# Kernel tuning notes

Hardware: AMD Instinct MI355X
Metric: run time of the kernel (lower is better)

Reference implementation:

```python
import jax, jax.numpy as jnp
import numpy as np

D_MODEL = 1024
H = 16
D_K = D_MODEL // H
THETA = 10000.0
MAX_SEQ = 2048
SEQ = 2048
BATCH = 2


def _rope_tables():
    # tri[i, k] angles: i / theta**(2k/d_k)
    pos = jnp.arange(MAX_SEQ, dtype=jnp.float32)[:, None]          # [S, 1]
    inv_freq = THETA ** (-2.0 * jnp.arange(D_K // 2, dtype=jnp.float32) / D_K)  # [dk/2]
    ang = pos * inv_freq                                            # [S, dk/2]
    return jnp.cos(ang), jnp.sin(ang)


def _apply_rope(x, token_positions, cos_t, sin_t):
    # x: [b, h, s, dk]; rotate interleaved pairs
    cos = cos_t[token_positions]  # [s, dk/2]
    sin = sin_t[token_positions]
    x2 = x.reshape(x.shape[:-1] + (D_K // 2, 2))
    x0, x1 = x2[..., 0], x2[..., 1]
    r0 = x0 * cos - x1 * sin
    r1 = x0 * sin + x1 * cos
    return jnp.stack([r0, r1], axis=-1).reshape(x.shape)


def setup_inputs() -> dict:
    key = jax.random.key(0)
    ks = jax.random.split(key, 5)
    sigma = np.sqrt(2.0 / (D_MODEL + D_MODEL))
    return {
        "x": jax.random.normal(ks[0], (BATCH, SEQ, D_MODEL), dtype=jnp.float32),
        "token_positions": jnp.arange(SEQ, dtype=jnp.int64 if jax.config.jax_enable_x64 else jnp.int32),
        "Wq": (jax.random.normal(ks[1], (D_MODEL, D_MODEL), dtype=jnp.float32) * sigma),
        "Wk": (jax.random.normal(ks[2], (D_MODEL, D_MODEL), dtype=jnp.float32) * sigma),
        "Wv": (jax.random.normal(ks[3], (D_MODEL, D_MODEL), dtype=jnp.float32) * sigma),
        "Wo": (jax.random.normal(ks[4], (D_MODEL, D_MODEL), dtype=jnp.float32) * sigma),
    }


def reference(x, token_positions, Wq, Wk, Wv, Wo):
    b, s, _ = x.shape
    cos_t, sin_t = _rope_tables()

    def proj(W):
        y = jnp.einsum('oi,bsi->bso', W, x)                 # [b, s, d_model]
        return y.reshape(b, s, H, D_K).transpose(0, 2, 1, 3)  # [b, h, s, dk]

    Q = _apply_rope(proj(Wq), token_positions, cos_t, sin_t)
    K = _apply_rope(proj(Wk), token_positions, cos_t, sin_t)
    V = proj(Wv)

    scores = jnp.einsum('bhqd,bhkd->bhqk', Q, K) / jnp.sqrt(jnp.float32(D_K))
    causal = jnp.tril(jnp.ones((s, s), dtype=bool))
    scores = jnp.where(causal, scores, -jnp.inf)
    attn = jax.nn.softmax(scores, axis=-1)
    out = jnp.einsum('bhqk,bhkd->bhqd', attn, V)            # [b, h, s, dv]
    out = out.transpose(0, 2, 1, 3).reshape(b, s, D_MODEL)
    return jnp.einsum('oi,bsi->bso', Wo, out)
```

## Files before the change

### kernel.cpp

```cpp
#include <hip/hip_runtime.h>
#include <hip/hip_bf16.h>
#include <math.h>

#define D_MODEL 1024
#define NH      16
#define DK      64
#define SEQ     2048
#define BATCH   2

typedef float  f32x4  __attribute__((ext_vector_type(4)));
typedef __bf16 bf16x8 __attribute__((ext_vector_type(8)));
typedef unsigned short ushx4 __attribute__((ext_vector_type(4)));
typedef unsigned short ushx8 __attribute__((ext_vector_type(8)));
typedef unsigned short u16;

__device__ inline u16 cbf(float f) { __bf16 h = (__bf16)f; return *(u16*)&h; }

__device__ inline void gload16(const u16* g, u16* l) {
    __builtin_amdgcn_global_load_lds(
        (const __attribute__((address_space(1))) unsigned int*)g,
        (__attribute__((address_space(3))) unsigned int*)l,
        16, 0, 0);
}

__global__ void rope_tables_kernel(float2* __restrict__ cs) {
    int i = blockIdx.x * 256 + threadIdx.x;
    int pos = i >> 5, k = i & 31;
    float inv = powf(10000.0f, -2.0f * (float)k / 64.0f);
    float ang = (float)pos * inv;
    cs[i] = make_float2(cosf(ang), sinf(ang));
}

__global__ void cvt_kernel(const float* __restrict__ in, u16* __restrict__ out) {
    size_t i = ((size_t)blockIdx.x * 256 + threadIdx.x) * 8;
    f32x4 v0 = *(const f32x4*)(in + i);
    f32x4 v1 = *(const f32x4*)(in + i + 4);
    ushx4 o0, o1;
    #pragma unroll
    for (int e = 0; e < 4; e++) { o0[e] = cbf(v0[e]); o1[e] = cbf(v1[e]); }
    *(ushx4*)(out + i) = o0;
    *(ushx4*)(out + i + 4) = o1;
}

__global__ void cvtw_kernel(const float* __restrict__ wq, const float* __restrict__ wk,
                            const float* __restrict__ wv, const float* __restrict__ wo,
                            u16* __restrict__ oq, u16* __restrict__ ok,
                            u16* __restrict__ ov, u16* __restrict__ oo) {
    const float* in; u16* out;
    switch (blockIdx.y) {
        case 0: in = wq; out = oq; break;
        case 1: in = wk; out = ok; break;
        case 2: in = wv; out = ov; break;
        default: in = wo; out = oo; break;
    }
    size_t i = ((size_t)blockIdx.x * 256 + threadIdx.x) * 8;
    f32x4 v0 = *(const f32x4*)(in + i);
    f32x4 v1 = *(const f32x4*)(in + i + 4);
    ushx4 o0, o1;
    #pragma unroll
    for (int e = 0; e < 4; e++) { o0[e] = cbf(v0[e]); o1[e] = cbf(v1[e]); }
    *(ushx4*)(out + i) = o0;
    *(ushx4*)(out + i + 4) = o1;
}

template<int MODE>
__global__ __launch_bounds__(256) void gemm_bt(
    const u16* __restrict__ A, const u16* __restrict__ W,
    u16* __restrict__ Qo, u16* __restrict__ Ko, void* __restrict__ Oo,
    const int* __restrict__ tpos, const float2* __restrict__ cs)
{
    constexpr int K = 1024;
    __shared__ u16 As[2][128 * 32];
    __shared__ u16 Bs[2][128 * 32];

    const int t  = threadIdx.x;
    const int m0 = blockIdx.x * 128, n0 = blockIdx.y * 128;
    const int lane = t & 63, wid = t >> 6;
    const int wm = wid >> 1, wn = wid & 1;
    const int lr = lane & 15, lg = lane >> 4;

    const int ldrow0 = wid * 32 + (lane >> 2);
    const int ldrow1 = ldrow0 + 16;
    const int lc = lane & 3;
    const u16* Asrc0 = A + (size_t)(m0 + ldrow0) * K + ((lc ^ ((ldrow0 >> 1) & 3)) << 3);
    const u16* Asrc1 = A + (size_t)(m0 + ldrow1) * K + ((lc ^ ((ldrow1 >> 1) & 3)) << 3);
    const u16* Bsrc0 = W + (size_t)(n0 + ldrow0) * K + ((lc ^ ((ldrow0 >> 1) & 3)) << 3);
    const u16* Bsrc1 = W + (size_t)(n0 + ldrow1) * K + ((lc ^ ((ldrow1 >> 1) & 3)) << 3);
    const int d0 = (wid * 32) * 32, d1 = (wid * 32 + 16) * 32;

    f32x4 acc[4][4];
    #pragma unroll
    for (int i = 0; i < 4; i++)
        #pragma unroll
        for (int j2 = 0; j2 < 4; j2++) acc[i][j2] = 0.0f;

    auto stage = [&](int buf, int k0) {
        gload16(Asrc0 + k0, &As[buf][d0]);
        gload16(Asrc1 + k0, &As[buf][d1]);
        gload16(Bsrc0 + k0, &Bs[buf][d0]);
        gload16(Bsrc1 + k0, &Bs[buf][d1]);
    };

    stage(0, 0);
    int buf = 0;
    for (int k0 = 0; k0 < K; k0 += 32) {
        __syncthreads();
        if (k0 + 32 < K) stage(buf ^ 1, k0 + 32);

        bf16x8 af[4], bfr[4];
        #pragma unroll
        for (int mi = 0; mi < 4; mi++) {
            int row = wm * 64 + mi * 16 + lr;
            af[mi] = *(const bf16x8*)&As[buf][row * 32 + ((lg ^ ((row >> 1) & 3)) << 3)];
        }
        #pragma unroll
        for (int ni = 0; ni < 4; ni++) {
            int row = wn * 64 + ni * 16 + lr;
            bfr[ni] = *(const bf16x8*)&Bs[buf][row * 32 + ((lg ^ ((row >> 1) & 3)) << 3)];
        }
        #pragma unroll
        for (int mi = 0; mi < 4; mi++)
            #pragma unroll
            for (int ni = 0; ni < 4; ni++) {
                if constexpr (MODE == 3)
                    acc[mi][ni] = __builtin_amdgcn_mfma_f32_16x16x32_bf16(bfr[ni], af[mi], acc[mi][ni], 0, 0, 0);
                else
                    acc[mi][ni] = __builtin_amdgcn_mfma_f32_16x16x32_bf16(af[mi], bfr[ni], acc[mi][ni], 0, 0, 0);
            }
        buf ^= 1;
    }

    #pragma unroll
    for (int mi = 0; mi < 4; mi++)
        #pragma unroll
        for (int ni = 0; ni < 4; ni++) {
            f32x4 v4 = acc[mi][ni];
            #pragma unroll
            for (int r = 0; r < 4; r++) {
                float v = v4[r];
                if constexpr (MODE == 3) {
                    int n = n0 + wn * 64 + ni * 16 + lg * 4 + r;
                    int m = m0 + wm * 64 + mi * 16 + lr;
                    int h = n >> 6, d = n & 63;
                    int b = m >> 11, s = m & 2047;
                    ((u16*)Oo)[(((size_t)b * NH + h) * DK + d) * SEQ + s] = cbf(v);
                } else {
                    int m = m0 + wm * 64 + mi * 16 + lg * 4 + r;
                    int n = n0 + wn * 64 + ni * 16 + lr;
                    if constexpr (MODE == 2) {
                        ((float*)Oo)[(size_t)m * D_MODEL + n] = v;
                    } else {
                        int b = m >> 11, s = m & 2047;
                        int h = (n >> 6) & 15, d = n & 63;
                        float vp = __shfl_xor(v, 1);
                        int tp = tpos[s];
                        float2 c2 = cs[tp * 32 + (d >> 1)];
                        float res = (d & 1) ? (vp * c2.y + v * c2.x) : (v * c2.x - vp * c2.y);
                        const int sel = n0 >> 10;
                        if (sel == 0) res *= 0.18033688f;
                        u16* outp = sel ? Ko : Qo;
                        outp[(((size_t)b * NH + h) * SEQ + s) * DK + d] = cbf(res);
                    }
                }
            }
        }
}

__global__ __launch_bounds__(256) void attn_kernel(
    const u16* __restrict__ Q,
    const u16* __restrict__ Km,
    const u16* __restrict__ VT,
    u16* __restrict__ aout)
{
    __shared__ u16 Ks[2][64 * 64];
    __shared__ u16 Vs[64 * 64];
    __shared__ u16 Pl[4][16 * 64];
    const int t = threadIdx.x, wid = t >> 6, lane = t & 63;
    const int lr = lane & 15, lg = lane >> 4;
    const int bx = blockIdx.x;
    const int j = bx & 31;
    const int qb = 31 - (bx >> 5);
    const int bh = (j & 7) * 4 + (j >> 3);
    const int b = bh >> 4, h = bh & 15;
    const int q0 = qb * 64;
    const int qw = q0 + wid * 16;
    const int nkt = qb + 1;
    const int srow = lane >> 3, schunk = lane & 7;

    const u16* Qg = Q  + (size_t)bh * SEQ * DK;
    const u16* Kg = Km + (size_t)bh * SEQ * DK;
    const u16* Vg = VT + (size_t)bh * DK * SEQ;
    u16* Plw = Pl[wid];

    bf16x8 aq[2];
    #pragma unroll
    for (int h2 = 0; h2 < 2; h2++)
        aq[h2] = *(const bf16x8*)&Qg[(qw + lr) * DK + h2 * 32 + lg * 8];

    float m_run = -__builtin_inff(), l_run = 0.0f;
    f32x4 acc[4];
    #pragma unroll
    for (int dg = 0; dg < 4; dg++) acc[dg] = 0.0f;

    auto stageK = [&](int buf, int kb) {
        const int row0 = wid * 16;
        const u16* ks = Kg + (size_t)(kb + row0 + srow) * DK + ((schunk ^ srow) << 3);
        gload16(ks,          &Ks[buf][row0 * 64]);
        gload16(ks + 8 * DK, &Ks[buf][(row0 + 8) * 64]);
    };
    auto stageV = [&](int kb) {
        const int row0 = wid * 16;
        const u16* vs = Vg + (size_t)(row0 + srow) * SEQ + kb + ((schunk ^ srow) << 3);
        gload16(vs,                   &Vs[row0 * 64]);
        gload16(vs + (size_t)8 * SEQ, &Vs[(row0 + 8) * 64]);
    };

    stageK(0, 0);
    for (int kt = 0; kt < nkt; kt++) {
        __builtin_amdgcn_sched_barrier(0);
        __builtin_amdgcn_s_barrier();
        __builtin_amdgcn_sched_barrier(0);
        stageV(kt * 64);
        stageK((kt + 1) & 1, (kt + 1 < nkt) ? (kt + 1) * 64 : 0);
        const int kb = kt * 64;

        asm volatile("s_waitcnt vmcnt(4)" ::: "memory");
        __builtin_amdgcn_sched_barrier(0);
        bf16x8 kf[4][2];
        #pragma unroll
        for (int kg = 0; kg < 4; kg++)
            #pragma unroll
            for (int h2 = 0; h2 < 2; h2++) {
                int row = kg * 16 + lr;
                kf[kg][h2] = *(const bf16x8*)&Ks[kt & 1][row * 64 + (((h2 * 4 + lg) ^ (lr & 7)) << 3)];
            }

        f32x4 sf[4];
        #pragma unroll
        for (int kg = 0; kg < 4; kg++) sf[kg] = 0.0f;
        __builtin_amdgcn_s_setprio(1);
        #pragma unroll
        for (int kg = 0; kg < 4; kg++) {
            sf[kg] = __builtin_amdgcn_mfma_f32_16x16x32_bf16(kf[kg][0], aq[0], sf[kg], 0, 0, 0);
            sf[kg] = __builtin_amdgcn_mfma_f32_16x16x32_bf16(kf[kg][1], aq[1], sf[kg], 0, 0, 0);
        }
        __builtin_amdgcn_s_setprio(0);

        {
            if (kb + 64 > qw) {
                const int qq = qw + lr;
                #pragma unroll
                for (int kg = 0; kg < 4; kg++)
                    #pragma unroll
                    for (int r = 0; r < 4; r++)
                        if (kb + kg * 16 + lg * 4 + r > qq) sf[kg][r] = -__builtin_inff();
            }
            float cmax = sf[0][0];
            #pragma unroll
            for (int kg = 0; kg < 4; kg++)
                #pragma unroll
                for (int r = 0; r < 4; r++) cmax = fmaxf(cmax, sf[kg][r]);
            if (!__all(cmax <= m_run + 8.0f)) {
                float mt = fmaxf(cmax, __shfl_xor(cmax, 16));
                mt = fmaxf(mt, __shfl_xor(mt, 32));
                float mn = fmaxf(m_run, mt);
                float scr = exp2f(m_run - mn);
                m_run = mn;
                l_run *= scr;
                #pragma unroll
                for (int dg = 0; dg < 4; dg++) acc[dg] *= scr;
            }
            float l = 0.0f;
            const int prow = lr * 64;
            #pragma unroll
            for (int kg = 0; kg < 4; kg++) {
                ushx4 pk;
                #pragma unroll
                for (int r = 0; r < 4; r++) {
                    float p = exp2f(sf[kg][r] - m_run);
                    l += p;
                    pk[r] = cbf(p);
                }
                *(ushx4*)&Plw[prow + (((kg * 4 + lg) ^ ((lr & 7) << 1)) << 2)] = pk;
            }
            l_run += l;
        }

        asm volatile("s_waitcnt vmcnt(2)" ::: "memory");
        __builtin_amdgcn_sched_barrier(0);
        bf16x8 vf[2][4];
        #pragma unroll
        for (int ck = 0; ck < 2; ck++)
            #pragma unroll
            for (int dg = 0; dg < 4; dg++) {
                int row = dg * 16 + lr;
                vf[ck][dg] = *(const bf16x8*)&Vs[row * 64 + (((ck * 4 + lg) ^ (lr & 7)) << 3)];
            }

        asm volatile("s_waitcnt lgkmcnt(0)" ::: "memory");
        __builtin_amdgcn_sched_barrier(0);
        bf16x8 pa[2];
        #pragma unroll
        for (int ck = 0; ck < 2; ck++)
            pa[ck] = *(const bf16x8*)&Plw[lr * 64 + (((ck * 8 + lg * 2) ^ ((lr & 7) << 1)) << 2)];
        __builtin_amdgcn_s_setprio(1);
        #pragma unroll
        for (int ck = 0; ck < 2; ck++)
            #pragma unroll
            for (int dg = 0; dg < 4; dg++)
                acc[dg] = __builtin_amdgcn_mfma_f32_16x16x32_bf16(vf[ck][dg], pa[ck], acc[dg], 0, 0, 0);
        __builtin_amdgcn_s_setprio(0);
    }

    l_run += __shfl_xor(l_run, 16);
    l_run += __shfl_xor(l_run, 32);

    {
        float inv = 1.0f / l_run;
        int q = qw + lr;
        #pragma unroll
        for (int dg = 0; dg < 4; dg++) {
            ushx4 ow;
            #pragma unroll
            for (int r = 0; r < 4; r++) ow[r] = cbf(acc[dg][r] * inv);
            *(ushx4*)&aout[((size_t)b * SEQ + q) * D_MODEL + h * DK + dg * 16 + lg * 4] = ow;
        }
    }
}

extern "C" void kernel_launch(void* const* d_in, const int* in_sizes, int n_in,
                              void* d_out, int out_size, void* d_ws, size_t ws_size,
                              hipStream_t stream) {
    const float* x    = (const float*)d_in[0];
    const int*   tpos = (const int*)d_in[1];
    const float* Wq   = (const float*)d_in[2];
    const float* Wk   = (const float*)d_in[3];
    const float* Wv   = (const float*)d_in[4];
    const float* Wo   = (const float*)d_in[5];
    float* out = (float*)d_out;

    char* ws = (char*)d_ws;
    float2* cs = (float2*)ws;
    u16* Qb   = (u16*)(ws + (512 << 10));
    u16* Kb   = (u16*)(ws + (512 << 10) + ((size_t)8  << 20));
    u16* VT   = (u16*)(ws + (512 << 10) + ((size_t)16 << 20));
    u16* xb   = (u16*)(ws + (512 << 10) + ((size_t)24 << 20));
    u16* Wqb  = (u16*)(ws + (512 << 10) + ((size_t)32 << 20));
    u16* Wkb  = (u16*)(ws + (512 << 10) + ((size_t)34 << 20));
    u16* Wvb  = (u16*)(ws + (512 << 10) + ((size_t)36 << 20));
    u16* Wob  = (u16*)(ws + (512 << 10) + ((size_t)38 << 20));
    u16* attnb = xb;

    rope_tables_kernel<<<256, 256, 0, stream>>>(cs);
    cvt_kernel<<<2048, 256, 0, stream>>>(x, xb);
    cvtw_kernel<<<dim3(512, 4), 256, 0, stream>>>(Wq, Wk, Wv, Wo, Wqb, Wkb, Wvb, Wob);

    gemm_bt<0><<<dim3(32, 16), 256, 0, stream>>>(xb, Wqb, Qb, Kb, nullptr, tpos, cs);
    gemm_bt<3><<<dim3(32, 8),  256, 0, stream>>>(xb, Wvb, nullptr, nullptr, VT, tpos, cs);

    attn_kernel<<<1024, 256, 0, stream>>>(Qb, Kb, VT, attnb);

    gemm_bt<2><<<dim3(32, 8),  256, 0, stream>>>(attnb, Wob, nullptr, nullptr, out, tpos, cs);
}
```

Baseline: 131.1 us.

## Pair complementary causal query blocks per workgroup to balance attention work

The attention grid is halved to 512 blocks, and each block now processes two query tiles, 31-p and p, so every block does the same total number of key tiles under the causal mask. This removes the load imbalance and tail of the longest-first schedule. Pointer increments also replace the per-tile address recomputation in the staging lambdas. The cost is fewer concurrent blocks, which means less latency hiding per CU, and the two tiles in a block run one after the other.

```diff
diff --git a/kernel.cpp b/kernel.cpp
--- a/kernel.cpp
+++ b/kernel.cpp
@@ -179,153 +179,161 @@
     const int lr = lane & 15, lg = lane >> 4;
     const int bx = blockIdx.x;
     const int j = bx & 31;
-    const int qb = 31 - (bx >> 5);
+    const int p = bx >> 5;
     const int bh = (j & 7) * 4 + (j >> 3);
     const int b = bh >> 4, h = bh & 15;
-    const int q0 = qb * 64;
-    const int qw = q0 + wid * 16;
-    const int nkt = qb + 1;
     const int srow = lane >> 3, schunk = lane & 7;
+    const int row0 = wid * 16;
+    const int swz = (schunk ^ srow) << 3;
 
     const u16* Qg = Q  + (size_t)bh * SEQ * DK;
     const u16* Kg = Km + (size_t)bh * SEQ * DK;
     const u16* Vg = VT + (size_t)bh * DK * SEQ;
     u16* Plw = Pl[wid];
 
-    bf16x8 aq[2];
-    #pragma unroll
-    for (int h2 = 0; h2 < 2; h2++)
-        aq[h2] = *(const bf16x8*)&Qg[(qw + lr) * DK + h2 * 32 + lg * 8];
-
-    float m_run = -__builtin_inff(), l_run = 0.0f;
-    f32x4 acc[4];
-    #pragma unroll
-    for (int dg = 0; dg < 4; dg++) acc[dg] = 0.0f;
-
-    auto stageK = [&](int buf, int kb) {
-        const int row0 = wid * 16;
-        const u16* ks = Kg + (size_t)(kb + row0 + srow) * DK + ((schunk ^ srow) << 3);
-        gload16(ks,          &Ks[buf][row0 * 64]);
-        gload16(ks + 8 * DK, &Ks[buf][(row0 + 8) * 64]);
-    };
-    auto stageV = [&](int kb) {
-        const int row0 = wid * 16;
-        const u16* vs = Vg + (size_t)(row0 + srow) * SEQ + kb + ((schunk ^ srow) << 3);
-        gload16(vs,                   &Vs[row0 * 64]);
-        gload16(vs + (size_t)8 * SEQ, &Vs[(row0 + 8) * 64]);
-    };
-
-    stageK(0, 0);
-    for (int kt = 0; kt < nkt; kt++) {
-        __builtin_amdgcn_sched_barrier(0);
-        __builtin_amdgcn_s_barrier();
-        __builtin_amdgcn_sched_barrier(0);
-        stageV(kt * 64);
-        stageK((kt + 1) & 1, (kt + 1 < nkt) ? (kt + 1) * 64 : 0);
-        const int kb = kt * 64;
-
-        asm volatile("s_waitcnt vmcnt(4)" ::: "memory");
-        __builtin_amdgcn_sched_barrier(0);
-        bf16x8 kf[4][2];
-        #pragma unroll
-        for (int kg = 0; kg < 4; kg++)
-            #pragma unroll
-            for (int h2 = 0; h2 < 2; h2++) {
-                int row = kg * 16 + lr;
-                kf[kg][h2] = *(const bf16x8*)&Ks[kt & 1][row * 64 + (((h2 * 4 + lg) ^ (lr & 7)) << 3)];
-            }
-
-        f32x4 sf[4];
-        #pragma unroll
-        for (int kg = 0; kg < 4; kg++) sf[kg] = 0.0f;
-        __builtin_amdgcn_s_setprio(1);
-        #pragma unroll
-        for (int kg = 0; kg < 4; kg++) {
-            sf[kg] = __builtin_amdgcn_mfma_f32_16x16x32_bf16(kf[kg][0], aq[0], sf[kg], 0, 0, 0);
-            sf[kg] = __builtin_amdgcn_mfma_f32_16x16x32_bf16(kf[kg][1], aq[1], sf[kg], 0, 0, 0);
-        }
-        __builtin_amdgcn_s_setprio(0);
-
-        {
-            if (kb + 64 > qw) {
-                const int qq = qw + lr;
+    auto process = [&](int qb) {
+        const int q0 = qb * 64;
+        const int qw = q0 + row0;
+        const int nkt = qb + 1;
+
+        __syncthreads();
+
+        bf16x8 aq[2];
+        #pragma unroll
+        for (int h2 = 0; h2 < 2; h2++)
+            aq[h2] = *(const bf16x8*)&Qg[(qw + lr) * DK + h2 * 32 + lg * 8];
+
+        float m_run = -__builtin_inff(), l_run = 0.0f;
+        f32x4 acc[4];
+        #pragma unroll
+        for (int dg = 0; dg < 4; dg++) acc[dg] = 0.0f;
+
+        const u16* kptr = Kg + (size_t)(row0 + srow) * DK + swz;
+        const u16* vptr = Vg + (size_t)(row0 + srow) * SEQ + swz;
+
+        gload16(kptr,          &Ks[0][row0 * 64]);
+        gload16(kptr + 8 * DK, &Ks[0][(row0 + 8) * 64]);
+        kptr += 64 * DK;
+
+        for (int kt = 0; kt < nkt; kt++) {
+            __builtin_amdgcn_sched_barrier(0);
+            __builtin_amdgcn_s_barrier();
+            __builtin_amdgcn_sched_barrier(0);
+            gload16(vptr,                   &Vs[row0 * 64]);
+            gload16(vptr + (size_t)8 * SEQ, &Vs[(row0 + 8) * 64]);
+            vptr += 64;
+            u16* kd = &Ks[(kt + 1) & 1][0];
+            gload16(kptr,          kd + row0 * 64);
+            gload16(kptr + 8 * DK, kd + (row0 + 8) * 64);
+            kptr += 64 * DK;
+            const int kb = kt * 64;
+
+            asm volatile("s_waitcnt vmcnt(4)" ::: "memory");
+            __builtin_amdgcn_sched_barrier(0);
+            bf16x8 kf[4][2];
+            #pragma unroll
+            for (int kg = 0; kg < 4; kg++)
+                #pragma unroll
+                for (int h2 = 0; h2 < 2; h2++) {
+                    int row = kg * 16 + lr;
+                    kf[kg][h2] = *(const bf16x8*)&Ks[kt & 1][row * 64 + (((h2 * 4 + lg) ^ (lr & 7)) << 3)];
+                }
+
+            f32x4 sf[4];
+            #pragma unroll
+            for (int kg = 0; kg < 4; kg++) sf[kg] = 0.0f;
+            __builtin_amdgcn_s_setprio(1);
+            #pragma unroll
+            for (int kg = 0; kg < 4; kg++) {
+                sf[kg] = __builtin_amdgcn_mfma_f32_16x16x32_bf16(kf[kg][0], aq[0], sf[kg], 0, 0, 0);
+                sf[kg] = __builtin_amdgcn_mfma_f32_16x16x32_bf16(kf[kg][1], aq[1], sf[kg], 0, 0, 0);
+            }
+            __builtin_amdgcn_s_setprio(0);
+
+            {
+                if (kb + 64 > qw) {
+                    const int qq = qw + lr;
+                    #pragma unroll
+                    for (int kg = 0; kg < 4; kg++)
+                        #pragma unroll
+                        for (int r = 0; r < 4; r++)
+                            if (kb + kg * 16 + lg * 4 + r > qq) sf[kg][r] = -__builtin_inff();
+                }
+                float cmax = sf[0][0];
                 #pragma unroll
                 for (int kg = 0; kg < 4; kg++)
                     #pragma unroll
-                    for (int r = 0; r < 4; r++)
-                        if (kb + kg * 16 + lg * 4 + r > qq) sf[kg][r] = -__builtin_inff();
-            }
-            float cmax = sf[0][0];
-            #pragma unroll
-            for (int kg = 0; kg < 4; kg++)
-                #pragma unroll
-                for (int r = 0; r < 4; r++) cmax = fmaxf(cmax, sf[kg][r]);
-            if (!__all(cmax <= m_run + 8.0f)) {
-                float mt = fmaxf(cmax, __shfl_xor(cmax, 16));
-                mt = fmaxf(mt, __shfl_xor(mt, 32));
-                float mn = fmaxf(m_run, mt);
-                float scr = exp2f(m_run - mn);
-                m_run = mn;
-                l_run *= scr;
-                #pragma unroll
-                for (int dg = 0; dg < 4; dg++) acc[dg] *= scr;
-            }
-            float l = 0.0f;
-            const int prow = lr * 64;
-            #pragma unroll
-            for (int kg = 0; kg < 4; kg++) {
-                ushx4 pk;
-                #pragma unroll
-                for (int r = 0; r < 4; r++) {
-                    float p = exp2f(sf[kg][r] - m_run);
-                    l += p;
-                    pk[r] = cbf(p);
-                }
-                *(ushx4*)&Plw[prow + (((kg * 4 + lg) ^ ((lr & 7) << 1)) << 2)] = pk;
-            }
-            l_run += l;
-        }
-
-        asm volatile("s_waitcnt vmcnt(2)" ::: "memory");
-        __builtin_amdgcn_sched_barrier(0);
-        bf16x8 vf[2][4];
-        #pragma unroll
-        for (int ck = 0; ck < 2; ck++)
+                    for (int r = 0; r < 4; r++) cmax = fmaxf(cmax, sf[kg][r]);
+                if (!__all(cmax <= m_run + 8.0f)) {
+                    float mt = fmaxf(cmax, __shfl_xor(cmax, 16));
+                    mt = fmaxf(mt, __shfl_xor(mt, 32));
+                    float mn = fmaxf(m_run, mt);
+                    float scr = exp2f(m_run - mn);
+                    m_run = mn;
+                    l_run *= scr;
+                    #pragma unroll
+                    for (int dg = 0; dg < 4; dg++) acc[dg] *= scr;
+                }
+                float l = 0.0f;
+                const int prow = lr * 64;
+                #pragma unroll
+                for (int kg = 0; kg < 4; kg++) {
+                    ushx4 pk;
+                    #pragma unroll
+                    for (int r = 0; r < 4; r++) {
+                        float pv = exp2f(sf[kg][r] - m_run);
+                        l += pv;
+                        pk[r] = cbf(pv);
+                    }
+                    *(ushx4*)&Plw[prow + (((kg * 4 + lg) ^ ((lr & 7) << 1)) << 2)] = pk;
+                }
+                l_run += l;
+            }
+
+            asm volatile("s_waitcnt vmcnt(2)" ::: "memory");
+            __builtin_amdgcn_sched_barrier(0);
+            bf16x8 vf[2][4];
+            #pragma unroll
+            for (int ck = 0; ck < 2; ck++)
+                #pragma unroll
+                for (int dg = 0; dg < 4; dg++) {
+                    int row = dg * 16 + lr;
+                    vf[ck][dg] = *(const bf16x8*)&Vs[row * 64 + (((ck * 4 + lg) ^ (lr & 7)) << 3)];
+                }
+
+            asm volatile("s_waitcnt lgkmcnt(0)" ::: "memory");
+            __builtin_amdgcn_sched_barrier(0);
+            bf16x8 pa[2];
+            #pragma unroll
+            for (int ck = 0; ck < 2; ck++)
+                pa[ck] = *(const bf16x8*)&Plw[lr * 64 + (((ck * 8 + lg * 2) ^ ((lr & 7) << 1)) << 2)];
+            __builtin_amdgcn_s_setprio(1);
+            #pragma unroll
+            for (int ck = 0; ck < 2; ck++)
+                #pragma unroll
+                for (int dg = 0; dg < 4; dg++)
+                    acc[dg] = __builtin_amdgcn_mfma_f32_16x16x32_bf16(vf[ck][dg], pa[ck], acc[dg], 0, 0, 0);
+            __builtin_amdgcn_s_setprio(0);
+        }
+
+        l_run += __shfl_xor(l_run, 16);
+        l_run += __shfl_xor(l_run, 32);
+
+        {
+            float inv = 1.0f / l_run;
+            int q = qw + lr;
             #pragma unroll
             for (int dg = 0; dg < 4; dg++) {
-                int row = dg * 16 + lr;
-                vf[ck][dg] = *(const bf16x8*)&Vs[row * 64 + (((ck * 4 + lg) ^ (lr & 7)) << 3)];
-            }
-
-        asm volatile("s_waitcnt lgkmcnt(0)" ::: "memory");
-        __builtin_amdgcn_sched_barrier(0);
-        bf16x8 pa[2];
-        #pragma unroll
-        for (int ck = 0; ck < 2; ck++)
-            pa[ck] = *(const bf16x8*)&Plw[lr * 64 + (((ck * 8 + lg * 2) ^ ((lr & 7) << 1)) << 2)];
-        __builtin_amdgcn_s_setprio(1);
-        #pragma unroll
-        for (int ck = 0; ck < 2; ck++)
-            #pragma unroll
-            for (int dg = 0; dg < 4; dg++)
-                acc[dg] = __builtin_amdgcn_mfma_f32_16x16x32_bf16(vf[ck][dg], pa[ck], acc[dg], 0, 0, 0);
-        __builtin_amdgcn_s_setprio(0);
-    }
-
-    l_run += __shfl_xor(l_run, 16);
-    l_run += __shfl_xor(l_run, 32);
-
-    {
-        float inv = 1.0f / l_run;
-        int q = qw + lr;
-        #pragma unroll
-        for (int dg = 0; dg < 4; dg++) {
-            ushx4 ow;
-            #pragma unroll
-            for (int r = 0; r < 4; r++) ow[r] = cbf(acc[dg][r] * inv);
-            *(ushx4*)&aout[((size_t)b * SEQ + q) * D_MODEL + h * DK + dg * 16 + lg * 4] = ow;
-        }
-    }
+                ushx4 ow;
+                #pragma unroll
+                for (int r = 0; r < 4; r++) ow[r] = cbf(acc[dg][r] * inv);
+                *(ushx4*)&aout[((size_t)b * SEQ + q) * D_MODEL + h * DK + dg * 16 + lg * 4] = ow;
+            }
+        }
+    };
+
+    process(31 - p);
+    process(p);
 }
 
 extern "C" void kernel_launch(void* const* d_in, const int* in_sizes, int n_in,
@@ -358,7 +366,7 @@
     gemm_bt<0><<<dim3(32, 16), 256, 0, stream>>>(xb, Wqb, Qb, Kb, nullptr, tpos, cs);
     gemm_bt<3><<<dim3(32, 8),  256, 0, stream>>>(xb, Wvb, nullptr, nullptr, VT, tpos, cs);
 
-    attn_kernel<<<1024, 256, 0, stream>>>(Qb, Kb, VT, attnb);
+    attn_kernel<<<512, 256, 0, stream>>>(Qb, Kb, VT, attnb);
 
     gemm_bt<2><<<dim3(32, 8),  256, 0, stream>>>(attnb, Wob, nullptr, nullptr, out, tpos, cs);
 }
```

New measurement: 134.1 us. 1.02x slower.

## Fuse prep kernels and software-pipeline PV MFMA with double-buffered V

Applied to the files above, without the earlier changes.

Merges the rope-table, activation-convert and weight-convert kernels into a single prep launch to cut launch overhead. In the attention kernel, V is now double-buffered and the P·V MFMAs for tile kt-1 are deferred into iteration kt, right after the QK^T MFMAs. The softmax of the current tile can then overlap with the previous PV matmul and the V load latency is hidden. The cost is twice the V LDS footprint, carrying the P fragments in registers across iterations, and an epilogue that drains the final tile.

```diff
diff --git a/kernel.cpp b/kernel.cpp
--- a/kernel.cpp
+++ b/kernel.cpp
@@ -23,44 +23,43 @@
         16, 0, 0);
 }
 
-__global__ void rope_tables_kernel(float2* __restrict__ cs) {
-    int i = blockIdx.x * 256 + threadIdx.x;
-    int pos = i >> 5, k = i & 31;
-    float inv = powf(10000.0f, -2.0f * (float)k / 64.0f);
-    float ang = (float)pos * inv;
-    cs[i] = make_float2(cosf(ang), sinf(ang));
-}
-
-__global__ void cvt_kernel(const float* __restrict__ in, u16* __restrict__ out) {
-    size_t i = ((size_t)blockIdx.x * 256 + threadIdx.x) * 8;
-    f32x4 v0 = *(const f32x4*)(in + i);
-    f32x4 v1 = *(const f32x4*)(in + i + 4);
-    ushx4 o0, o1;
-    #pragma unroll
-    for (int e = 0; e < 4; e++) { o0[e] = cbf(v0[e]); o1[e] = cbf(v1[e]); }
-    *(ushx4*)(out + i) = o0;
-    *(ushx4*)(out + i + 4) = o1;
-}
-
-__global__ void cvtw_kernel(const float* __restrict__ wq, const float* __restrict__ wk,
+__global__ void prep_kernel(const float* __restrict__ x,
+                            const float* __restrict__ wq, const float* __restrict__ wk,
                             const float* __restrict__ wv, const float* __restrict__ wo,
-                            u16* __restrict__ oq, u16* __restrict__ ok,
-                            u16* __restrict__ ov, u16* __restrict__ oo) {
-    const float* in; u16* out;
-    switch (blockIdx.y) {
-        case 0: in = wq; out = oq; break;
-        case 1: in = wk; out = ok; break;
-        case 2: in = wv; out = ov; break;
-        default: in = wo; out = oo; break;
-    }
-    size_t i = ((size_t)blockIdx.x * 256 + threadIdx.x) * 8;
-    f32x4 v0 = *(const f32x4*)(in + i);
-    f32x4 v1 = *(const f32x4*)(in + i + 4);
-    ushx4 o0, o1;
-    #pragma unroll
-    for (int e = 0; e < 4; e++) { o0[e] = cbf(v0[e]); o1[e] = cbf(v1[e]); }
-    *(ushx4*)(out + i) = o0;
-    *(ushx4*)(out + i + 4) = o1;
+                            u16* __restrict__ xb,
+                            u16* __restrict__ wqb, u16* __restrict__ wkb,
+                            u16* __restrict__ wvb, u16* __restrict__ wob,
+                            float2* __restrict__ cs)
+{
+    const int bx = blockIdx.x, t = threadIdx.x;
+    if (bx < 4096) {
+        const float* in; u16* out; size_t base;
+        if (bx < 2048) { in = x; out = xb; base = (size_t)bx * 2048; }
+        else {
+            int i = bx - 2048, sel = i >> 9;
+            base = (size_t)(i & 511) * 2048;
+            switch (sel) {
+                case 0:  in = wq; out = wqb; break;
+                case 1:  in = wk; out = wkb; break;
+                case 2:  in = wv; out = wvb; break;
+                default: in = wo; out = wob; break;
+            }
+        }
+        size_t idx = base + (size_t)t * 8;
+        f32x4 v0 = *(const f32x4*)(in + idx);
+        f32x4 v1 = *(const f32x4*)(in + idx + 4);
+        ushx4 o0, o1;
+        #pragma unroll
+        for (int e = 0; e < 4; e++) { o0[e] = cbf(v0[e]); o1[e] = cbf(v1[e]); }
+        *(ushx4*)(out + idx) = o0;
+        *(ushx4*)(out + idx + 4) = o1;
+    } else {
+        int i = (bx - 4096) * 256 + t;
+        int pos = i >> 5, k = i & 31;
+        float inv = powf(10000.0f, -2.0f * (float)k / 64.0f);
+        float ang = (float)pos * inv;
+        cs[i] = make_float2(cosf(ang), sinf(ang));
+    }
 }
 
 template<int MODE>
@@ -173,7 +172,7 @@
     u16* __restrict__ aout)
 {
     __shared__ u16 Ks[2][64 * 64];
-    __shared__ u16 Vs[64 * 64];
+    __shared__ u16 Vs[2][64 * 64];
     __shared__ u16 Pl[4][16 * 64];
     const int t = threadIdx.x, wid = t >> 6, lane = t & 63;
     const int lr = lane & 15, lg = lane >> 4;
@@ -183,9 +182,11 @@
     const int bh = (j & 7) * 4 + (j >> 3);
     const int b = bh >> 4, h = bh & 15;
     const int q0 = qb * 64;
-    const int qw = q0 + wid * 16;
+    const int row0 = wid * 16;
+    const int qw = q0 + row0;
     const int nkt = qb + 1;
     const int srow = lane >> 3, schunk = lane & 7;
+    const int swz = (schunk ^ srow) << 3;
 
     const u16* Qg = Q  + (size_t)bh * SEQ * DK;
     const u16* Kg = Km + (size_t)bh * SEQ * DK;
@@ -201,18 +202,17 @@
     f32x4 acc[4];
     #pragma unroll
     for (int dg = 0; dg < 4; dg++) acc[dg] = 0.0f;
+    bf16x8 paR[2];
 
     auto stageK = [&](int buf, int kb) {
-        const int row0 = wid * 16;
-        const u16* ks = Kg + (size_t)(kb + row0 + srow) * DK + ((schunk ^ srow) << 3);
+        const u16* ks = Kg + (size_t)(kb + row0 + srow) * DK + swz;
         gload16(ks,          &Ks[buf][row0 * 64]);
         gload16(ks + 8 * DK, &Ks[buf][(row0 + 8) * 64]);
     };
-    auto stageV = [&](int kb) {
-        const int row0 = wid * 16;
-        const u16* vs = Vg + (size_t)(row0 + srow) * SEQ + kb + ((schunk ^ srow) << 3);
-        gload16(vs,                   &Vs[row0 * 64]);
-        gload16(vs + (size_t)8 * SEQ, &Vs[(row0 + 8) * 64]);
+    auto stageV = [&](int buf, int kb) {
+        const u16* vs = Vg + (size_t)(row0 + srow) * SEQ + kb + swz;
+        gload16(vs,                   &Vs[buf][row0 * 64]);
+        gload16(vs + (size_t)8 * SEQ, &Vs[buf][(row0 + 8) * 64]);
     };
 
     stageK(0, 0);
@@ -220,7 +220,7 @@
         __builtin_amdgcn_sched_barrier(0);
         __builtin_amdgcn_s_barrier();
         __builtin_amdgcn_sched_barrier(0);
-        stageV(kt * 64);
+        stageV(kt & 1, kt * 64);
         stageK((kt + 1) & 1, (kt + 1 < nkt) ? (kt + 1) * 64 : 0);
         const int kb = kt * 64;
 
@@ -245,6 +245,20 @@
             sf[kg] = __builtin_amdgcn_mfma_f32_16x16x32_bf16(kf[kg][1], aq[1], sf[kg], 0, 0, 0);
         }
         __builtin_amdgcn_s_setprio(0);
+
+        if (kt) {
+            const int vb = (kt - 1) & 1;
+            __builtin_amdgcn_s_setprio(1);
+            #pragma unroll
+            for (int ck = 0; ck < 2; ck++)
+                #pragma unroll
+                for (int dg = 0; dg < 4; dg++) {
+                    int row = dg * 16 + lr;
+                    bf16x8 vf = *(const bf16x8*)&Vs[vb][row * 64 + (((ck * 4 + lg) ^ (lr & 7)) << 3)];
+                    acc[dg] = __builtin_amdgcn_mfma_f32_16x16x32_bf16(vf, paR[ck], acc[dg], 0, 0, 0);
+                }
+            __builtin_amdgcn_s_setprio(0);
+        }
 
         {
             if (kb + 64 > qw) {
@@ -277,38 +291,35 @@
                 ushx4 pk;
                 #pragma unroll
                 for (int r = 0; r < 4; r++) {
-                    float p = exp2f(sf[kg][r] - m_run);
-                    l += p;
-                    pk[r] = cbf(p);
+                    float pv = exp2f(sf[kg][r] - m_run);
+                    l += pv;
+                    pk[r] = cbf(pv);
                 }
                 *(ushx4*)&Plw[prow + (((kg * 4 + lg) ^ ((lr & 7) << 1)) << 2)] = pk;
             }
             l_run += l;
         }
 
-        asm volatile("s_waitcnt vmcnt(2)" ::: "memory");
+        asm volatile("s_waitcnt lgkmcnt(0)" ::: "memory");
         __builtin_amdgcn_sched_barrier(0);
-        bf16x8 vf[2][4];
+        #pragma unroll
+        for (int ck = 0; ck < 2; ck++)
+            paR[ck] = *(const bf16x8*)&Plw[lr * 64 + (((ck * 8 + lg * 2) ^ ((lr & 7) << 1)) << 2)];
+    }
+
+    asm volatile("s_waitcnt vmcnt(2)" ::: "memory");
+    __builtin_amdgcn_sched_barrier(0);
+    {
+        const int vb = (nkt - 1) & 1;
+        __builtin_amdgcn_s_setprio(1);
         #pragma unroll
         for (int ck = 0; ck < 2; ck++)
             #pragma unroll
             for (int dg = 0; dg < 4; dg++) {
                 int row = dg * 16 + lr;
-                vf[ck][dg] = *(const bf16x8*)&Vs[row * 64 + (((ck * 4 + lg) ^ (lr & 7)) << 3)];
-            }
-
-        asm volatile("s_waitcnt lgkmcnt(0)" ::: "memory");
-        __builtin_amdgcn_sched_barrier(0);
-        bf16x8 pa[2];
-        #pragma unroll
-        for (int ck = 0; ck < 2; ck++)
-            pa[ck] = *(const bf16x8*)&Plw[lr * 64 + (((ck * 8 + lg * 2) ^ ((lr & 7) << 1)) << 2)];
-        __builtin_amdgcn_s_setprio(1);
-        #pragma unroll
-        for (int ck = 0; ck < 2; ck++)
-            #pragma unroll
-            for (int dg = 0; dg < 4; dg++)
-                acc[dg] = __builtin_amdgcn_mfma_f32_16x16x32_bf16(vf[ck][dg], pa[ck], acc[dg], 0, 0, 0);
+                bf16x8 vf = *(const bf16x8*)&Vs[vb][row * 64 + (((ck * 4 + lg) ^ (lr & 7)) << 3)];
+                acc[dg] = __builtin_amdgcn_mfma_f32_16x16x32_bf16(vf, paR[ck], acc[dg], 0, 0, 0);
+            }
         __builtin_amdgcn_s_setprio(0);
     }
 
@@ -351,9 +362,7 @@
     u16* Wob  = (u16*)(ws + (512 << 10) + ((size_t)38 << 20));
     u16* attnb = xb;
 
-    rope_tables_kernel<<<256, 256, 0, stream>>>(cs);
-    cvt_kernel<<<2048, 256, 0, stream>>>(x, xb);
-    cvtw_kernel<<<dim3(512, 4), 256, 0, stream>>>(Wq, Wk, Wv, Wo, Wqb, Wkb, Wvb, Wob);
+    prep_kernel<<<4352, 256, 0, stream>>>(x, Wq, Wk, Wv, Wo, xb, Wqb, Wkb, Wvb, Wob, cs);
 
     gemm_bt<0><<<dim3(32, 16), 256, 0, stream>>>(xb, Wqb, Qb, Kb, nullptr, tpos, cs);
     gemm_bt<3><<<dim3(32, 8),  256, 0, stream>>>(xb, Wvb, nullptr, nullptr, VT, tpos, cs);
```

After: 123.7 us. 5.7% less time.
